# Kernel optimization log

Hardware: AMD Instinct MI355X
Metric: run time of the kernel (lower is better)

The kernel has to match this reference:

```python
import jax, jax.numpy as jnp
import numpy as np

DIM = 512
H = 8
D = 64
EPS = 1e-5


def _ln(x, g, b):
    m = jnp.mean(x, axis=-1, keepdims=True)
    v = jnp.var(x, axis=-1, keepdims=True)
    return (x - m) * jax.lax.rsqrt(v + EPS) * g + b


def _attn(x, ctx, wq, wk, wv, wo, bo):
    B, S, _ = x.shape
    T = ctx.shape[1]
    q = (x @ wq).reshape(B, S, H, D)
    k = (ctx @ wk).reshape(B, T, H, D)
    v = (ctx @ wv).reshape(B, T, H, D)
    scale = D ** -0.5
    score = jnp.einsum('bqhd,bkhd->bhqk', q, k) * scale  # [B,H,S,T]
    w = jax.nn.softmax(score, axis=-1)
    o = jnp.einsum('bhqk,bkhd->bqhd', w, v).reshape(B, S, H * D)
    return o @ wo + bo


def _geglu(x, w, b):
    h = x @ w + b
    y, gate = h[..., :4 * DIM], h[..., 4 * DIM:]
    tanh_res = jnp.tanh(gate * 0.7978845608 * (1.0 + 0.044715 * gate * gate))
    return y * 0.5 * gate * (1.0 + tanh_res)


def setup_inputs() -> dict:
    key = jax.random.key(0)
    ks = jax.random.split(key, 16)
    s = 0.02
    inp = {
        'x': jax.random.normal(ks[0], (2, 4096, DIM), jnp.float32),
        'context': jax.random.normal(ks[1], (2, 77, DIM), jnp.float32),
        'ln1_g': jnp.ones((DIM,), jnp.float32),
        'ln1_b': jnp.zeros((DIM,), jnp.float32),
        'wq1': jax.random.normal(ks[2], (DIM, H * D), jnp.float32) * s,
        'wk1': jax.random.normal(ks[3], (DIM, H * D), jnp.float32) * s,
        'wv1': jax.random.normal(ks[4], (DIM, H * D), jnp.float32) * s,
        'wo1': jax.random.normal(ks[5], (H * D, H * D), jnp.float32) * s,
        'bo1': jnp.zeros((H * D,), jnp.float32),
        'ln2_g': jnp.ones((DIM,), jnp.float32),
        'ln2_b': jnp.zeros((DIM,), jnp.float32),
        'wq2': jax.random.normal(ks[6], (DIM, H * D), jnp.float32) * s,
        'wk2': jax.random.normal(ks[7], (DIM, H * D), jnp.float32) * s,
        'wv2': jax.random.normal(ks[8], (DIM, H * D), jnp.float32) * s,
        'wo2': jax.random.normal(ks[9], (H * D, H * D), jnp.float32) * s,
        'bo2': jnp.zeros((H * D,), jnp.float32),
        'ln3_g': jnp.ones((DIM,), jnp.float32),
        'ln3_b': jnp.zeros((DIM,), jnp.float32),
        'geglu_w': jax.random.normal(ks[10], (DIM, 8 * DIM), jnp.float32) * s,
        'geglu_b': jnp.zeros((8 * DIM,), jnp.float32),
        'out_w': jax.random.normal(ks[11], (4 * DIM, DIM), jnp.float32) * s,
        'out_b': jnp.zeros((DIM,), jnp.float32),
    }
    return inp


def reference(x, context, ln1_g, ln1_b, wq1, wk1, wv1, wo1, bo1,
              ln2_g, ln2_b, wq2, wk2, wv2, wo2, bo2,
              ln3_g, ln3_b, geglu_w, geglu_b, out_w, out_b):
    h = _attn(_ln(x, ln1_g, ln1_b), _ln(x, ln1_g, ln1_b), wq1, wk1, wv1, wo1, bo1) + x
    h = _attn(_ln(h, ln2_g, ln2_b), context, wq2, wk2, wv2, wo2, bo2) + h
    ff = _geglu(_ln(h, ln3_g, ln3_b), geglu_w, geglu_b)
    return ff @ out_w + out_b + h
```

## Files before the change

kernel.cpp:

```cpp
#include <hip/hip_runtime.h>
#include <hip/hip_bf16.h>
#include <math.h>

#define DIM 512
#define NHEAD 8
#define HD 64
#define BATCH 2
#define SEQ 4096
#define CTXLEN 77
#define NTOK (BATCH*SEQ)
#define NCTX (BATCH*CTXLEN)

typedef __hip_bfloat16 bf16;
typedef __attribute__((ext_vector_type(8))) short bf8_t;
typedef __attribute__((ext_vector_type(4))) float f4_t;

__device__ __forceinline__ float b2f(bf16 v){ return __bfloat162float(v); }
__device__ __forceinline__ bf16  f2b(float v){ return __float2bfloat16(v); }
__device__ __forceinline__ unsigned short f2bu(float v){ bf16 h = f2b(v); return *(unsigned short*)&h; }
__device__ __forceinline__ unsigned int packbf2(float a, float b){
    unsigned int au = __float_as_uint(a) + 0x8000u;
    unsigned int bu = __float_as_uint(b) + 0x8000u;
    return __builtin_amdgcn_perm(bu, au, 0x07060302u);
}
__device__ __forceinline__ void  stf(float* p, float v){ *p = v; }
__device__ __forceinline__ void  stf(bf16* p, float v){ *p = f2b(v); }

__global__ __launch_bounds__(256)
void ln_kernel(const float* __restrict__ x, const float* __restrict__ g,
               const float* __restrict__ b, bf16* __restrict__ out, int nrows)
{
    int row  = blockIdx.x * 4 + (threadIdx.x >> 6);
    int lane = threadIdx.x & 63;
    if (row >= nrows) return;
    const float* xr = x + (size_t)row * DIM;
    float v[8];
    float s = 0.f, sq = 0.f;
    #pragma unroll
    for (int j = 0; j < 8; ++j) {
        float f = xr[lane + 64*j];
        v[j] = f; s += f; sq += f*f;
    }
    #pragma unroll
    for (int off = 32; off; off >>= 1) {
        s  += __shfl_xor(s,  off);
        sq += __shfl_xor(sq, off);
    }
    float mean = s * (1.f/DIM);
    float var  = sq * (1.f/DIM) - mean*mean;
    float rstd = rsqrtf(var + 1e-5f);
    bf16* orow = out + (size_t)row * DIM;
    #pragma unroll
    for (int j = 0; j < 8; ++j) {
        int c = lane + 64*j;
        orow[c] = f2b((v[j]-mean)*rstd*g[c] + b[c]);
    }
}

__global__ __launch_bounds__(256)
void transpose_bf16_kernel(const float* __restrict__ W, bf16* __restrict__ Wt, int K, int N)
{
    __shared__ float tile[32][33];
    int n0 = blockIdx.x * 32, k0 = blockIdx.y * 32;
    int tx = threadIdx.x & 31, ty = threadIdx.x >> 5;
    #pragma unroll
    for (int p = 0; p < 4; ++p)
        tile[ty + p*8][tx] = W[(size_t)(k0 + ty + p*8)*N + n0 + tx];
    __syncthreads();
    #pragma unroll
    for (int p = 0; p < 4; ++p)
        Wt[(size_t)(n0 + ty + p*8)*K + k0 + tx] = f2b(tile[tx][ty + p*8]);
}

struct TPtrs { const float* src[8]; bf16* dst[8]; };
__global__ __launch_bounds__(256)
void transpose8_kernel(TPtrs p)
{
    __shared__ float tile[32][33];
    const float* W = p.src[blockIdx.z];
    bf16* Wt = p.dst[blockIdx.z];
    int n0 = blockIdx.x * 32, k0 = blockIdx.y * 32;
    int tx = threadIdx.x & 31, ty = threadIdx.x >> 5;
    #pragma unroll
    for (int q = 0; q < 4; ++q)
        tile[ty + q*8][tx] = W[(size_t)(k0 + ty + q*8)*512 + n0 + tx];
    __syncthreads();
    #pragma unroll
    for (int q = 0; q < 4; ++q)
        Wt[(size_t)(n0 + ty + q*8)*512 + k0 + tx] = f2b(tile[tx][ty + q*8]);
}

__global__ __launch_bounds__(256)
void cast_bf16_kernel(const float* __restrict__ in, bf16* __restrict__ out, int n)
{
    int i = blockIdx.x*256 + threadIdx.x;
    if (i < n) out[i] = f2b(in[i]);
}

__global__ __launch_bounds__(256)
void v_transpose_kernel(const bf16* __restrict__ V, bf16* __restrict__ Vt, int T, int pitch)
{
    __shared__ __align__(16) unsigned short tile[64*64];
    const int tid = threadIdx.x;
    const int b = blockIdx.z, h = blockIdx.y;
    const int t0 = blockIdx.x * 64;
    #pragma unroll
    for (int it = 0; it < 2; ++it) {
        int e = tid + it*256;
        int t = e >> 3, c = e & 7;
        int gk = t0 + t;
        bf8_t v = {0,0,0,0,0,0,0,0};
        if (gk < T) v = *(const bf8_t*)(V + ((size_t)(b*T + gk))*DIM + h*HD + c*8);
        *(bf8_t*)&tile[t*64 + c*8] = v;
    }
    __syncthreads();
    #pragma unroll
    for (int it = 0; it < 2; ++it) {
        int e = tid + it*256;
        int d = e & 63, oc = e >> 6;
        unsigned short tmp[8];
        #pragma unroll
        for (int j = 0; j < 8; ++j) tmp[j] = tile[(oc*8 + j)*64 + d];
        *(bf8_t*)(Vt + ((size_t)((b*8 + h)*64 + d))*pitch + t0 + oc*8) = *(bf8_t*)tmp;
    }
}

struct OutPtrs { void* p[3]; };
template<int RESID, typename OUTT, bool GUARD>
__global__ __launch_bounds__(256)
void gemm_mfma_kernel(const bf16* __restrict__ A, const bf16* __restrict__ Wt,
                      const float* __restrict__ bias, const float* __restrict__ resid,
                      OutPtrs outs, int M, int K)
{
    __shared__ __align__(16) unsigned short As[128*64];
    __shared__ __align__(16) unsigned short Bs[64*64];
    const int tid  = threadIdx.x;
    const int wave = tid >> 6, lane = tid & 63;
    const int l16  = lane & 15, quad = lane >> 4;
    const int wm = (wave >> 1) * 64, wn = (wave & 1) * 32;
    const int m0 = blockIdx.y * 128, n0 = blockIdx.x * 64;
    OUTT* outp = (OUTT*)outs.p[n0 >> 9];
    const int lc0 = n0 & 511;
    const int sr = tid >> 3, sc_ = tid & 7;

    f4_t acc[4][2];
    #pragma unroll
    for (int i = 0; i < 4; ++i) { acc[i][0] = f4_t{0,0,0,0}; acc[i][1] = f4_t{0,0,0,0}; }

    bf8_t pa[4], pb[2];
    #pragma unroll
    for (int p = 0; p < 4; ++p) {
        int r = sr + p*32;
        int gr = m0 + r;
        if (GUARD) gr = (gr < M) ? gr : (M-1);
        pa[p] = *(const bf8_t*)(A + (size_t)gr*K + sc_*8);
    }
    #pragma unroll
    for (int p = 0; p < 2; ++p)
        pb[p] = *(const bf8_t*)(Wt + (size_t)(n0 + sr + p*32)*K + sc_*8);

    for (int k0 = 0; k0 < K; k0 += 64) {
        #pragma unroll
        for (int p = 0; p < 4; ++p) {
            int r = sr + p*32;
            *(bf8_t*)&As[r*64 + ((sc_ ^ (r&7))*8)] = pa[p];
        }
        #pragma unroll
        for (int p = 0; p < 2; ++p) {
            int r = sr + p*32;
            *(bf8_t*)&Bs[r*64 + ((sc_ ^ (r&7))*8)] = pb[p];
        }
        __syncthreads();
        if (k0 + 64 < K) {
            #pragma unroll
            for (int p = 0; p < 4; ++p) {
                int r = sr + p*32;
                int gr = m0 + r;
                if (GUARD) gr = (gr < M) ? gr : (M-1);
                pa[p] = *(const bf8_t*)(A + (size_t)gr*K + k0 + 64 + sc_*8);
            }
            #pragma unroll
            for (int p = 0; p < 2; ++p)
                pb[p] = *(const bf8_t*)(Wt + (size_t)(n0 + sr + p*32)*K + k0 + 64 + sc_*8);
        }
        #pragma unroll
        for (int kc = 0; kc < 2; ++kc) {
            const int cg = kc*4 + quad;
            bf8_t af[4], bfr[2];
            #pragma unroll
            for (int mt = 0; mt < 4; ++mt) {
                int r = wm + mt*16 + l16;
                af[mt] = *(const bf8_t*)&As[r*64 + ((cg ^ (r&7))*8)];
            }
            #pragma unroll
            for (int nt = 0; nt < 2; ++nt) {
                int r = wn + nt*16 + l16;
                bfr[nt] = *(const bf8_t*)&Bs[r*64 + ((cg ^ (r&7))*8)];
            }
            #pragma unroll
            for (int mt = 0; mt < 4; ++mt)
                #pragma unroll
                for (int nt = 0; nt < 2; ++nt)
                    acc[mt][nt] = __builtin_amdgcn_mfma_f32_16x16x32_bf16(af[mt], bfr[nt], acc[mt][nt], 0, 0, 0);
        }
        __syncthreads();
    }

    #pragma unroll
    for (int mt = 0; mt < 4; ++mt) {
        #pragma unroll
        for (int r_ = 0; r_ < 4; ++r_) {
            int row = m0 + wm + mt*16 + quad*4 + r_;
            if (GUARD && row >= M) continue;
            size_t rb = (size_t)row * 512;
            #pragma unroll
            for (int nt = 0; nt < 2; ++nt) {
                int col = lc0 + wn + nt*16 + l16;
                float v = acc[mt][nt][r_];
                if (bias) v += bias[col];
                if (RESID) v += resid[rb + col];
                stf(&outp[rb + col], v);
            }
        }
    }
}

__global__ __launch_bounds__(256)
void geglu_mfma_kernel(const bf16* __restrict__ A, const bf16* __restrict__ WtG,
                       const float* __restrict__ bias, bf16* __restrict__ outp)
{
    __shared__ __align__(16) unsigned short As[128*64];
    __shared__ __align__(16) unsigned short Bys[64*64];
    __shared__ __align__(16) unsigned short Bgs[64*64];
    const int tid  = threadIdx.x;
    const int wave = tid >> 6, lane = tid & 63;
    const int l16  = lane & 15, quad = lane >> 4;
    const int m0 = blockIdx.y * 128, n0 = blockIdx.x * 64;
    const int sr = tid >> 3, sc_ = tid & 7;

    f4_t accy[2][4], accg[2][4];
    #pragma unroll
    for (int i = 0; i < 2; ++i)
        #pragma unroll
        for (int j = 0; j < 4; ++j) { accy[i][j] = f4_t{0,0,0,0}; accg[i][j] = f4_t{0,0,0,0}; }

    bf8_t pa[4], py[2], pg[2];
    #pragma unroll
    for (int p = 0; p < 4; ++p)
        pa[p] = *(const bf8_t*)(A + (size_t)(m0 + sr + p*32)*DIM + sc_*8);
    #pragma unroll
    for (int p = 0; p < 2; ++p) {
        py[p] = *(const bf8_t*)(WtG + (size_t)(n0 + sr + p*32)*DIM + sc_*8);
        pg[p] = *(const bf8_t*)(WtG + (size_t)(2048 + n0 + sr + p*32)*DIM + sc_*8);
    }

    for (int k0 = 0; k0 < DIM; k0 += 64) {
        #pragma unroll
        for (int p = 0; p < 4; ++p) {
            int r = sr + p*32;
            *(bf8_t*)&As[r*64 + ((sc_ ^ (r&7))*8)] = pa[p];
        }
        #pragma unroll
        for (int p = 0; p < 2; ++p) {
            int r = sr + p*32;
            *(bf8_t*)&Bys[r*64 + ((sc_ ^ (r&7))*8)] = py[p];
            *(bf8_t*)&Bgs[r*64 + ((sc_ ^ (r&7))*8)] = pg[p];
        }
        __syncthreads();
        if (k0 + 64 < DIM) {
            #pragma unroll
            for (int p = 0; p < 4; ++p)
                pa[p] = *(const bf8_t*)(A + (size_t)(m0 + sr + p*32)*DIM + k0 + 64 + sc_*8);
            #pragma unroll
            for (int p = 0; p < 2; ++p) {
                py[p] = *(const bf8_t*)(WtG + (size_t)(n0 + sr + p*32)*DIM + k0 + 64 + sc_*8);
                pg[p] = *(const bf8_t*)(WtG + (size_t)(2048 + n0 + sr + p*32)*DIM + k0 + 64 + sc_*8);
            }
        }
        #pragma unroll
        for (int kc = 0; kc < 2; ++kc) {
            const int cg = kc*4 + quad;
            bf8_t af[2];
            #pragma unroll
            for (int mt = 0; mt < 2; ++mt) {
                int r = wave*32 + mt*16 + l16;
                af[mt] = *(const bf8_t*)&As[r*64 + ((cg ^ (r&7))*8)];
            }
            #pragma unroll
            for (int nt = 0; nt < 4; ++nt) {
                int r = nt*16 + l16;
                bf8_t by = *(const bf8_t*)&Bys[r*64 + ((cg ^ (r&7))*8)];
                bf8_t bg = *(const bf8_t*)&Bgs[r*64 + ((cg ^ (r&7))*8)];
                #pragma unroll
                for (int mt = 0; mt < 2; ++mt) {
                    accy[mt][nt] = __builtin_amdgcn_mfma_f32_16x16x32_bf16(af[mt], by, accy[mt][nt], 0, 0, 0);
                    accg[mt][nt] = __builtin_amdgcn_mfma_f32_16x16x32_bf16(af[mt], bg, accg[mt][nt], 0, 0, 0);
                }
            }
        }
        __syncthreads();
    }

    #pragma unroll
    for (int mt = 0; mt < 2; ++mt) {
        #pragma unroll
        for (int r_ = 0; r_ < 4; ++r_) {
            int row = m0 + wave*32 + mt*16 + quad*4 + r_;
            size_t rb = (size_t)row * 2048;
            #pragma unroll
            for (int nt = 0; nt < 4; ++nt) {
                int col = n0 + nt*16 + l16;
                float y = accy[mt][nt][r_] + bias[col];
                float g = accg[mt][nt][r_] + bias[2048 + col];
                float t = tanhf(0.7978845608f*g*(1.f + 0.044715f*g*g));
                outp[rb + col] = f2b(y * 0.5f * g * (1.f + t));
            }
        }
    }
}

__global__ __launch_bounds__(256)
void attn_mfma_kernel(const bf16* __restrict__ Qm, const bf16* __restrict__ Km,
                      const bf16* __restrict__ VtG, bf16* __restrict__ Om,
                      int T, int vpitch)
{
    __shared__ __align__(16) unsigned short Ks[64*64];
    __shared__ __align__(16) unsigned short Vts[64*64];
    __shared__ __align__(16) unsigned short Ps[4][16*64];

    const int tid  = threadIdx.x;
    const int wave = tid >> 6, lane = tid & 63;
    const int l16  = lane & 15, quad = lane >> 4;
    const int b = blockIdx.z, h = blockIdx.y;
    const int qblk = blockIdx.x * 128;
    const int sr = tid >> 3, sc_ = tid & 7;

    bf8_t ones;
    #pragma unroll
    for (int j = 0; j < 8; ++j) ((unsigned short*)&ones)[j] = 0x3F80;

    bf8_t qf[2][2];
    #pragma unroll
    for (int qn = 0; qn < 2; ++qn) {
        const bf16* qp = Qm + ((size_t)(b*SEQ + qblk + wave*32 + qn*16 + l16))*DIM + h*HD + quad*8;
        #pragma unroll
        for (int kc = 0; kc < 2; ++kc) {
            bf8_t v = *(const bf8_t*)(qp + kc*32);
            unsigned short* u = (unsigned short*)&v;
            unsigned int* w = (unsigned int*)&v;
            #pragma unroll
            for (int j = 0; j < 4; ++j) {
                float f0 = b2f(*(bf16*)&u[2*j])   * 0.1803368801f;
                float f1 = b2f(*(bf16*)&u[2*j+1]) * 0.1803368801f;
                w[j] = packbf2(f0, f1);
            }
            qf[qn][kc] = v;
        }
    }

    f4_t o[4][2];
    #pragma unroll
    for (int dt = 0; dt < 4; ++dt) { o[dt][0] = f4_t{0,0,0,0}; o[dt][1] = f4_t{0,0,0,0}; }
    f4_t lacc[2] = {{0,0,0,0},{0,0,0,0}};

    bf8_t kq[2], vq[2];
    #pragma unroll
    for (int it = 0; it < 2; ++it) {
        int r = sr + it*32;
        kq[it] = bf8_t{0,0,0,0,0,0,0,0};
        if (r < T) kq[it] = *(const bf8_t*)(Km + ((size_t)(b*T + r))*DIM + h*HD + sc_*8);
        vq[it] = *(const bf8_t*)(VtG + ((size_t)((b*8 + h)*64 + r))*vpitch + sc_*8);
    }

    const int ntiles = (T + 63) >> 6;
    for (int t0 = 0; t0 < ntiles; ++t0) {
        const int kb = t0 << 6;
        #pragma unroll
        for (int it = 0; it < 2; ++it) {
            int r = sr + it*32;
            *(bf8_t*)&Ks[r*64 + ((sc_ ^ (r&7))*8)]  = kq[it];
            *(bf8_t*)&Vts[r*64 + ((sc_ ^ (r&7))*8)] = vq[it];
        }
        __syncthreads();
        if (t0 + 1 < ntiles) {
            int kbn = kb + 64;
            #pragma unroll
            for (int it = 0; it < 2; ++it) {
                int r = sr + it*32;
                int gk = kbn + r;
                kq[it] = bf8_t{0,0,0,0,0,0,0,0};
                if (gk < T) kq[it] = *(const bf8_t*)(Km + ((size_t)(b*T + gk))*DIM + h*HD + sc_*8);
                vq[it] = *(const bf8_t*)(VtG + ((size_t)((b*8 + h)*64 + r))*vpitch + kbn + sc_*8);
            }
        }

        bf8_t kf[4][2], vf[4][2];
        #pragma unroll
        for (int t = 0; t < 4; ++t) {
            int r = t*16 + l16;
            #pragma unroll
            for (int kc = 0; kc < 2; ++kc) {
                int cg = kc*4 + quad;
                kf[t][kc] = *(const bf8_t*)&Ks[r*64 + ((cg ^ (r&7))*8)];
                vf[t][kc] = *(const bf8_t*)&Vts[r*64 + ((cg ^ (r&7))*8)];
            }
        }
        const bool tail = (kb + 64 > T);

        #pragma unroll
        for (int qn = 0; qn < 2; ++qn) {
            f4_t sc[4];
            #pragma unroll
            for (int km = 0; km < 4; ++km) {
                f4_t c = {0,0,0,0};
                c = __builtin_amdgcn_mfma_f32_16x16x32_bf16(kf[km][0], qf[qn][0], c, 0, 0, 0);
                c = __builtin_amdgcn_mfma_f32_16x16x32_bf16(kf[km][1], qf[qn][1], c, 0, 0, 0);
                sc[km] = c;
            }
            if (tail) {
                #pragma unroll
                for (int km = 0; km < 4; ++km)
                    #pragma unroll
                    for (int r = 0; r < 4; ++r)
                        if (kb + km*16 + quad*4 + r >= T) sc[km][r] = -1e30f;
            }
            #pragma unroll
            for (int km = 0; km < 4; ++km) {
                uint2 w;
                w.x = packbf2(exp2f(sc[km][0]), exp2f(sc[km][1]));
                w.y = packbf2(exp2f(sc[km][2]), exp2f(sc[km][3]));
                int chunk = 2*km + (quad >> 1);
                int a = l16*64 + ((chunk ^ (l16 & 7))*8) + (quad & 1)*4;
                *(uint2*)&Ps[wave][a] = w;
            }
            #pragma unroll
            for (int kc = 0; kc < 2; ++kc) {
                int cg = kc*4 + quad;
                bf8_t pf = *(const bf8_t*)&Ps[wave][l16*64 + ((cg ^ (l16 & 7))*8)];
                lacc[qn] = __builtin_amdgcn_mfma_f32_16x16x32_bf16(ones, pf, lacc[qn], 0, 0, 0);
                #pragma unroll
                for (int dt = 0; dt < 4; ++dt)
                    o[dt][qn] = __builtin_amdgcn_mfma_f32_16x16x32_bf16(vf[dt][kc], pf, o[dt][qn], 0, 0, 0);
            }
        }
        __syncthreads();
    }

    #pragma unroll
    for (int qn = 0; qn < 2; ++qn) {
        float inv = 1.f / lacc[qn][0];
        int tok = qblk + wave*32 + qn*16 + l16;
        size_t base = ((size_t)(b*SEQ + tok))*DIM + h*HD;
        #pragma unroll
        for (int dt = 0; dt < 4; ++dt) {
            uint2 w;
            w.x = packbf2(o[dt][qn][0]*inv, o[dt][qn][1]*inv);
            w.y = packbf2(o[dt][qn][2]*inv, o[dt][qn][3]*inv);
            *(uint2*)(Om + base + dt*16 + quad*4) = w;
        }
    }
}

extern "C" void kernel_launch(void* const* d_in, const int* in_sizes, int n_in,
                              void* d_out, int out_size, void* d_ws, size_t ws_size,
                              hipStream_t stream)
{
    (void)in_sizes; (void)n_in; (void)out_size; (void)ws_size;
    const float* x    = (const float*)d_in[0];
    const float* ctx  = (const float*)d_in[1];
    const float* ln1g = (const float*)d_in[2];
    const float* ln1b = (const float*)d_in[3];
    const float* wq1  = (const float*)d_in[4];
    const float* wk1  = (const float*)d_in[5];
    const float* wv1  = (const float*)d_in[6];
    const float* wo1  = (const float*)d_in[7];
    const float* bo1  = (const float*)d_in[8];
    const float* ln2g = (const float*)d_in[9];
    const float* ln2b = (const float*)d_in[10];
    const float* wq2  = (const float*)d_in[11];
    const float* wk2  = (const float*)d_in[12];
    const float* wv2  = (const float*)d_in[13];
    const float* wo2  = (const float*)d_in[14];
    const float* bo2  = (const float*)d_in[15];
    const float* ln3g = (const float*)d_in[16];
    const float* ln3b = (const float*)d_in[17];
    const float* gw   = (const float*)d_in[18];
    const float* gb   = (const float*)d_in[19];
    const float* ow   = (const float*)d_in[20];
    const float* ob   = (const float*)d_in[21];
    float* out = (float*)d_out;

    char* ws = (char*)d_ws;
    bf16* An  = (bf16*)(ws);
    bf16* VtG = (bf16*)(ws);
    bf16* Qb  = (bf16*)(ws + ((size_t)8<<20));
    bf16* Kb  = (bf16*)(ws + ((size_t)16<<20));
    bf16* Vb  = (bf16*)(ws + ((size_t)24<<20));
    bf16* Ob  = (bf16*)(ws + ((size_t)32<<20));
    bf16* FF  = Qb;
    float* Hf = out;
    bf16* WT  = (bf16*)(ws + ((size_t)40<<20));
    bf16* wq1T = WT + 0*262144, *wk1T = WT + 1*262144, *wv1T = WT + 2*262144, *wo1T = WT + 3*262144;
    bf16* wq2T = WT + 4*262144, *wk2T = WT + 5*262144, *wv2T = WT + 6*262144, *wo2T = WT + 7*262144;
    bf16* gwT  = (bf16*)(ws + ((size_t)44<<20));
    bf16* owT  = (bf16*)(ws + ((size_t)48<<20));
    bf16* ctxb = (bf16*)(ws + ((size_t)50<<20));
    bf16* VtG2 = (bf16*)(ws + ((size_t)50<<20) + ((size_t)512<<10));

    dim3 blk(256);

    TPtrs tp;
    tp.src[0]=wq1; tp.src[1]=wk1; tp.src[2]=wv1; tp.src[3]=wo1;
    tp.src[4]=wq2; tp.src[5]=wk2; tp.src[6]=wv2; tp.src[7]=wo2;
    tp.dst[0]=wq1T; tp.dst[1]=wk1T; tp.dst[2]=wv1T; tp.dst[3]=wo1T;
    tp.dst[4]=wq2T; tp.dst[5]=wk2T; tp.dst[6]=wv2T; tp.dst[7]=wo2T;
    transpose8_kernel<<<dim3(16,16,8), blk, 0, stream>>>(tp);
    transpose_bf16_kernel<<<dim3(128,16), blk, 0, stream>>>(gw, gwT, DIM, 4096);
    transpose_bf16_kernel<<<dim3(16,64), blk, 0, stream>>>(ow, owT, 2048, DIM);
    cast_bf16_kernel<<<dim3((NCTX*DIM+255)/256), blk, 0, stream>>>(ctx, ctxb, NCTX*DIM);

    dim3 gLN(NTOK/4);
    dim3 gQKV(24, 64);
    dim3 gG(8, 64);
    dim3 gKVx(16, 2);
    dim3 gGEGLU(32, 64);
    dim3 gATT(SEQ/128, NHEAD, BATCH);
    OutPtrs oQKV{{Qb, Kb, Vb}};
    OutPtrs oKVx{{Kb, Vb, nullptr}};
    OutPtrs oQ{{Qb, nullptr, nullptr}};
    OutPtrs oH{{Hf, nullptr, nullptr}};
    OutPtrs oOut{{out, nullptr, nullptr}};

    ln_kernel<<<gLN, blk, 0, stream>>>(x, ln1g, ln1b, An, NTOK);
    gemm_mfma_kernel<0,bf16,false><<<gQKV, blk, 0, stream>>>(An, wq1T, nullptr, nullptr, oQKV, NTOK, DIM);
    v_transpose_kernel<<<dim3(SEQ/64, NHEAD, BATCH), blk, 0, stream>>>(Vb, VtG, SEQ, SEQ);
    attn_mfma_kernel<<<gATT, blk, 0, stream>>>(Qb, Kb, VtG, Ob, SEQ, SEQ);
    gemm_mfma_kernel<1,float,false><<<gG, blk, 0, stream>>>(Ob, wo1T, bo1, x, oH, NTOK, DIM);

    ln_kernel<<<gLN, blk, 0, stream>>>(Hf, ln2g, ln2b, An, NTOK);
    gemm_mfma_kernel<0,bf16,false><<<gG, blk, 0, stream>>>(An, wq2T, nullptr, nullptr, oQ, NTOK, DIM);
    gemm_mfma_kernel<0,bf16,true><<<gKVx, blk, 0, stream>>>(ctxb, wk2T, nullptr, nullptr, oKVx, NCTX, DIM);
    v_transpose_kernel<<<dim3(2, NHEAD, BATCH), blk, 0, stream>>>(Vb, VtG2, CTXLEN, 128);
    attn_mfma_kernel<<<gATT, blk, 0, stream>>>(Qb, Kb, VtG2, Ob, CTXLEN, 128);
    gemm_mfma_kernel<1,float,false><<<gG, blk, 0, stream>>>(Ob, wo2T, bo2, Hf, oH, NTOK, DIM);

    ln_kernel<<<gLN, blk, 0, stream>>>(Hf, ln3g, ln3b, An, NTOK);
    geglu_mfma_kernel<<<gGEGLU, blk, 0, stream>>>(An, gwT, gb, FF);
    gemm_mfma_kernel<1,float,false><<<gG, blk, 0, stream>>>(FF, owT, ob, Hf, oOut, NTOK, 2048);
}
```

Baseline: 518.7 us.

## Split attention block into 8 waves of 16 queries each

The attention kernel now runs 512 threads per block, with each of 8 waves handling 16 query rows instead of 4 waves handling 32. K/V tile staging is spread across twice as many threads, and per-wave register usage for accumulators and Q fragments is halved. This is meant to raise wave-level parallelism and latency hiding. In exchange, each wave reloads the full K/V fragments from LDS for half as many queries, doubling shared-memory read traffic per query, and the per-tile barriers now synchronize more waves.

```diff
diff --git a/kernel.cpp b/kernel.cpp
--- a/kernel.cpp
+++ b/kernel.cpp
@@ -319,14 +319,14 @@
     }
 }
 
-__global__ __launch_bounds__(256)
+__global__ __launch_bounds__(512)
 void attn_mfma_kernel(const bf16* __restrict__ Qm, const bf16* __restrict__ Km,
                       const bf16* __restrict__ VtG, bf16* __restrict__ Om,
                       int T, int vpitch)
 {
     __shared__ __align__(16) unsigned short Ks[64*64];
     __shared__ __align__(16) unsigned short Vts[64*64];
-    __shared__ __align__(16) unsigned short Ps[4][16*64];
+    __shared__ __align__(16) unsigned short Ps[8][16*64];
 
     const int tid  = threadIdx.x;
     const int wave = tid >> 6, lane = tid & 63;
@@ -339,10 +339,9 @@
     #pragma unroll
     for (int j = 0; j < 8; ++j) ((unsigned short*)&ones)[j] = 0x3F80;
 
-    bf8_t qf[2][2];
-    #pragma unroll
-    for (int qn = 0; qn < 2; ++qn) {
-        const bf16* qp = Qm + ((size_t)(b*SEQ + qblk + wave*32 + qn*16 + l16))*DIM + h*HD + quad*8;
+    bf8_t qf[2];
+    {
+        const bf16* qp = Qm + ((size_t)(b*SEQ + qblk + wave*16 + l16))*DIM + h*HD + quad*8;
         #pragma unroll
         for (int kc = 0; kc < 2; ++kc) {
             bf8_t v = *(const bf8_t*)(qp + kc*32);
@@ -354,44 +353,32 @@
                 float f1 = b2f(*(bf16*)&u[2*j+1]) * 0.1803368801f;
                 w[j] = packbf2(f0, f1);
             }
-            qf[qn][kc] = v;
-        }
-    }
-
-    f4_t o[4][2];
-    #pragma unroll
-    for (int dt = 0; dt < 4; ++dt) { o[dt][0] = f4_t{0,0,0,0}; o[dt][1] = f4_t{0,0,0,0}; }
-    f4_t lacc[2] = {{0,0,0,0},{0,0,0,0}};
-
-    bf8_t kq[2], vq[2];
-    #pragma unroll
-    for (int it = 0; it < 2; ++it) {
-        int r = sr + it*32;
-        kq[it] = bf8_t{0,0,0,0,0,0,0,0};
-        if (r < T) kq[it] = *(const bf8_t*)(Km + ((size_t)(b*T + r))*DIM + h*HD + sc_*8);
-        vq[it] = *(const bf8_t*)(VtG + ((size_t)((b*8 + h)*64 + r))*vpitch + sc_*8);
-    }
+            qf[kc] = v;
+        }
+    }
+
+    f4_t o[4];
+    #pragma unroll
+    for (int dt = 0; dt < 4; ++dt) o[dt] = f4_t{0,0,0,0};
+    f4_t lacc = {0,0,0,0};
+
+    bf8_t kq, vq;
+    kq = bf8_t{0,0,0,0,0,0,0,0};
+    if (sr < T) kq = *(const bf8_t*)(Km + ((size_t)(b*T + sr))*DIM + h*HD + sc_*8);
+    vq = *(const bf8_t*)(VtG + ((size_t)((b*8 + h)*64 + sr))*vpitch + sc_*8);
 
     const int ntiles = (T + 63) >> 6;
     for (int t0 = 0; t0 < ntiles; ++t0) {
         const int kb = t0 << 6;
-        #pragma unroll
-        for (int it = 0; it < 2; ++it) {
-            int r = sr + it*32;
-            *(bf8_t*)&Ks[r*64 + ((sc_ ^ (r&7))*8)]  = kq[it];
-            *(bf8_t*)&Vts[r*64 + ((sc_ ^ (r&7))*8)] = vq[it];
-        }
+        *(bf8_t*)&Ks[sr*64 + ((sc_ ^ (sr&7))*8)]  = kq;
+        *(bf8_t*)&Vts[sr*64 + ((sc_ ^ (sr&7))*8)] = vq;
         __syncthreads();
         if (t0 + 1 < ntiles) {
             int kbn = kb + 64;
-            #pragma unroll
-            for (int it = 0; it < 2; ++it) {
-                int r = sr + it*32;
-                int gk = kbn + r;
-                kq[it] = bf8_t{0,0,0,0,0,0,0,0};
-                if (gk < T) kq[it] = *(const bf8_t*)(Km + ((size_t)(b*T + gk))*DIM + h*HD + sc_*8);
-                vq[it] = *(const bf8_t*)(VtG + ((size_t)((b*8 + h)*64 + r))*vpitch + kbn + sc_*8);
-            }
+            int gk = kbn + sr;
+            kq = bf8_t{0,0,0,0,0,0,0,0};
+            if (gk < T) kq = *(const bf8_t*)(Km + ((size_t)(b*T + gk))*DIM + h*HD + sc_*8);
+            vq = *(const bf8_t*)(VtG + ((size_t)((b*8 + h)*64 + sr))*vpitch + kbn + sc_*8);
         }
 
         bf8_t kf[4][2], vf[4][2];
@@ -407,55 +394,51 @@
         }
         const bool tail = (kb + 64 > T);
 
-        #pragma unroll
-        for (int qn = 0; qn < 2; ++qn) {
-            f4_t sc[4];
-            #pragma unroll
-            for (int km = 0; km < 4; ++km) {
-                f4_t c = {0,0,0,0};
-                c = __builtin_amdgcn_mfma_f32_16x16x32_bf16(kf[km][0], qf[qn][0], c, 0, 0, 0);
-                c = __builtin_amdgcn_mfma_f32_16x16x32_bf16(kf[km][1], qf[qn][1], c, 0, 0, 0);
-                sc[km] = c;
-            }
-            if (tail) {
+        f4_t sc[4];
+        #pragma unroll
+        for (int km = 0; km < 4; ++km) {
+            f4_t c = {0,0,0,0};
+            c = __builtin_amdgcn_mfma_f32_16x16x32_bf16(kf[km][0], qf[0], c, 0, 0, 0);
+            c = __builtin_amdgcn_mfma_f32_16x16x32_bf16(kf[km][1], qf[1], c, 0, 0, 0);
+            sc[km] = c;
+        }
+        if (tail) {
+            #pragma unroll
+            for (int km = 0; km < 4; ++km)
                 #pragma unroll
-                for (int km = 0; km < 4; ++km)
-                    #pragma unroll
-                    for (int r = 0; r < 4; ++r)
-                        if (kb + km*16 + quad*4 + r >= T) sc[km][r] = -1e30f;
-            }
-            #pragma unroll
-            for (int km = 0; km < 4; ++km) {
-                uint2 w;
-                w.x = packbf2(exp2f(sc[km][0]), exp2f(sc[km][1]));
-                w.y = packbf2(exp2f(sc[km][2]), exp2f(sc[km][3]));
-                int chunk = 2*km + (quad >> 1);
-                int a = l16*64 + ((chunk ^ (l16 & 7))*8) + (quad & 1)*4;
-                *(uint2*)&Ps[wave][a] = w;
-            }
-            #pragma unroll
-            for (int kc = 0; kc < 2; ++kc) {
-                int cg = kc*4 + quad;
-                bf8_t pf = *(const bf8_t*)&Ps[wave][l16*64 + ((cg ^ (l16 & 7))*8)];
-                lacc[qn] = __builtin_amdgcn_mfma_f32_16x16x32_bf16(ones, pf, lacc[qn], 0, 0, 0);
-                #pragma unroll
-                for (int dt = 0; dt < 4; ++dt)
-                    o[dt][qn] = __builtin_amdgcn_mfma_f32_16x16x32_bf16(vf[dt][kc], pf, o[dt][qn], 0, 0, 0);
-            }
+                for (int r = 0; r < 4; ++r)
+                    if (kb + km*16 + quad*4 + r >= T) sc[km][r] = -1e30f;
+        }
+        #pragma unroll
+        for (int km = 0; km < 4; ++km) {
+            uint2 w;
+            w.x = packbf2(exp2f(sc[km][0]), exp2f(sc[km][1]));
+            w.y = packbf2(exp2f(sc[km][2]), exp2f(sc[km][3]));
+            int chunk = 2*km + (quad >> 1);
+            int a = l16*64 + ((chunk ^ (l16 & 7))*8) + (quad & 1)*4;
+            *(uint2*)&Ps[wave][a] = w;
+        }
+        #pragma unroll
+        for (int kc = 0; kc < 2; ++kc) {
+            int cg = kc*4 + quad;
+            bf8_t pf = *(const bf8_t*)&Ps[wave][l16*64 + ((cg ^ (l16 & 7))*8)];
+            lacc = __builtin_amdgcn_mfma_f32_16x16x32_bf16(ones, pf, lacc, 0, 0, 0);
+            #pragma unroll
+            for (int dt = 0; dt < 4; ++dt)
+                o[dt] = __builtin_amdgcn_mfma_f32_16x16x32_bf16(vf[dt][kc], pf, o[dt], 0, 0, 0);
         }
         __syncthreads();
     }
 
-    #pragma unroll
-    for (int qn = 0; qn < 2; ++qn) {
-        float inv = 1.f / lacc[qn][0];
-        int tok = qblk + wave*32 + qn*16 + l16;
+    {
+        float inv = 1.f / lacc[0];
+        int tok = qblk + wave*16 + l16;
         size_t base = ((size_t)(b*SEQ + tok))*DIM + h*HD;
         #pragma unroll
         for (int dt = 0; dt < 4; ++dt) {
             uint2 w;
-            w.x = packbf2(o[dt][qn][0]*inv, o[dt][qn][1]*inv);
-            w.y = packbf2(o[dt][qn][2]*inv, o[dt][qn][3]*inv);
+            w.x = packbf2(o[dt][0]*inv, o[dt][1]*inv);
+            w.y = packbf2(o[dt][2]*inv, o[dt][3]*inv);
             *(uint2*)(Om + base + dt*16 + quad*4) = w;
         }
     }
@@ -508,6 +491,7 @@
     bf16* VtG2 = (bf16*)(ws + ((size_t)50<<20) + ((size_t)512<<10));
 
     dim3 blk(256);
+    dim3 blkA(512);
 
     TPtrs tp;
     tp.src[0]=wq1; tp.src[1]=wk1; tp.src[2]=wv1; tp.src[3]=wo1;
@@ -534,14 +518,14 @@
     ln_kernel<<<gLN, blk, 0, stream>>>(x, ln1g, ln1b, An, NTOK);
     gemm_mfma_kernel<0,bf16,false><<<gQKV, blk, 0, stream>>>(An, wq1T, nullptr, nullptr, oQKV, NTOK, DIM);
     v_transpose_kernel<<<dim3(SEQ/64, NHEAD, BATCH), blk, 0, stream>>>(Vb, VtG, SEQ, SEQ);
-    attn_mfma_kernel<<<gATT, blk, 0, stream>>>(Qb, Kb, VtG, Ob, SEQ, SEQ);
+    attn_mfma_kernel<<<gATT, blkA, 0, stream>>>(Qb, Kb, VtG, Ob, SEQ, SEQ);
     gemm_mfma_kernel<1,float,false><<<gG, blk, 0, stream>>>(Ob, wo1T, bo1, x, oH, NTOK, DIM);
 
     ln_kernel<<<gLN, blk, 0, stream>>>(Hf, ln2g, ln2b, An, NTOK);
     gemm_mfma_kernel<0,bf16,false><<<gG, blk, 0, stream>>>(An, wq2T, nullptr, nullptr, oQ, NTOK, DIM);
     gemm_mfma_kernel<0,bf16,true><<<gKVx, blk, 0, stream>>>(ctxb, wk2T, nullptr, nullptr, oKVx, NCTX, DIM);
     v_transpose_kernel<<<dim3(2, NHEAD, BATCH), blk, 0, stream>>>(Vb, VtG2, CTXLEN, 128);
-    attn_mfma_kernel<<<gATT, blk, 0, stream>>>(Qb, Kb, VtG2, Ob, CTXLEN, 128);
+    attn_mfma_kernel<<<gATT, blkA, 0, stream>>>(Qb, Kb, VtG2, Ob, CTXLEN, 128);
     gemm_mfma_kernel<1,float,false><<<gG, blk, 0, stream>>>(Ob, wo2T, bo2, Hf, oH, NTOK, DIM);
 
     ln_kernel<<<gLN, blk, 0, stream>>>(Hf, ln3g, ln3b, An, NTOK);
```

After: 470.4 us. -9.3%, faster.
